# Kernel optimization log

Hardware: AMD Instinct MI355X
Metric: run time of the kernel (lower is better)

The kernel has to match this reference:

```python
import jax, jax.numpy as jnp
import numpy as np

B, N = 2048, 1024
ATOL, RTOL = 1e-6, 1e-3
MAX_STEPS = 40   # static bound on adaptive DOPRI5 steps over t in [0, 1]
DT0 = 0.1
T1 = 1.0

# Dormand-Prince 5(4) error coefficients (b5 - b4)
E1 = 71.0 / 57600.0
E3 = -71.0 / 16695.0
E4 = 71.0 / 1920.0
E5 = -17253.0 / 339200.0
E6 = 22.0 / 525.0
E7 = -1.0 / 40.0


def _dopri5_to_t1(f, y0):
    """Adaptive Dormand-Prince RK45 from t=0 to t=1 with a static step budget."""
    def body(carry, _):
        t, y, dt = carry
        done = t >= (T1 - 1e-7)
        h = jnp.where(done, jnp.float32(0.0), jnp.minimum(dt, T1 - t))
        k1 = f(y)
        k2 = f(y + h * (0.2 * k1))
        k3 = f(y + h * (3.0/40.0 * k1 + 9.0/40.0 * k2))
        k4 = f(y + h * (44.0/45.0 * k1 - 56.0/15.0 * k2 + 32.0/9.0 * k3))
        k5 = f(y + h * (19372.0/6561.0 * k1 - 25360.0/2187.0 * k2
                        + 64448.0/6561.0 * k3 - 212.0/729.0 * k4))
        k6 = f(y + h * (9017.0/3168.0 * k1 - 355.0/33.0 * k2 + 46732.0/5247.0 * k3
                        + 49.0/176.0 * k4 - 5103.0/18656.0 * k5))
        y5 = y + h * (35.0/384.0 * k1 + 500.0/1113.0 * k3 + 125.0/192.0 * k4
                      - 2187.0/6784.0 * k5 + 11.0/84.0 * k6)
        k7 = f(y5)  # FSAL stage, used only for error estimate here
        err = h * (E1*k1 + E3*k3 + E4*k4 + E5*k5 + E6*k6 + E7*k7)
        scale = ATOL + RTOL * jnp.maximum(jnp.abs(y), jnp.abs(y5))
        enorm = jnp.sqrt(jnp.mean(jnp.square(err / scale)))
        enorm = jnp.maximum(enorm, jnp.float32(1e-10))
        accept = enorm <= 1.0
        step_ok = jnp.logical_and(accept, jnp.logical_not(done))
        t_new = jnp.where(step_ok, t + h, t)
        y_new = jnp.where(step_ok, y5, y)
        factor = jnp.clip(0.9 * enorm ** (-0.2), 0.2, 5.0)
        dt_new = jnp.where(done, dt, dt * factor)
        return (t_new, y_new, dt_new), None

    carry0 = (jnp.float32(0.0), y0, jnp.float32(DT0))
    (_, y_final, _), _ = jax.lax.scan(jax.checkpoint(body), carry0, None, length=MAX_STEPS)
    return y_final


def setup_inputs() -> dict:
    key = jax.random.key(0)
    k1, k2, k3, k4 = jax.random.split(key, 4)
    inputs = jax.random.normal(k1, (B, N), dtype=jnp.float32)
    prev_state = jax.random.normal(k2, (B, N), dtype=jnp.float32)
    # keras initializers: tau='ones', weights/input_weights=RandomNormal(stddev=0.05), bias='zeros'
    tau = jnp.ones((N,), dtype=jnp.float32)
    weight_matrix = 0.05 * jax.random.normal(k3, (N, N), dtype=jnp.float32)
    input_weights = 0.05 * jax.random.normal(k4, (N,), dtype=jnp.float32)
    bias = jnp.zeros((N,), dtype=jnp.float32)
    return {"inputs": inputs, "prev_state": prev_state, "tau": tau,
            "weight_matrix": weight_matrix, "input_weights": input_weights, "bias": bias}


def reference(inputs, prev_state, tau, weight_matrix, input_weights, bias):
    drive = inputs * input_weights  # [B, N], constant over the integration
    inv_tau = 1.0 / tau

    def ode_fn(y):  # autonomous: dx/dt = (1/tau) * (-x + W @ tanh(x + b) + u * w_in)
        act = jnp.tanh(y + bias)
        rec = jnp.einsum('ij,bj->bi', weight_matrix, act)
        return inv_tau * (-y + rec + drive)

    new_state = _dopri5_to_t1(ode_fn, prev_state)
    return new_state
```

## Files before the change

### kernel.cpp

```cpp
#include <hip/hip_runtime.h>
#include <math.h>


typedef float f4 __attribute__((ext_vector_type(4)));
typedef float f32x4 __attribute__((ext_vector_type(4)));
typedef _Float16 half8v __attribute__((ext_vector_type(8)));
typedef _Float16 half2v __attribute__((ext_vector_type(2)));
typedef unsigned long long u64;

#define AS1 __attribute__((address_space(1)))
#define AS3 __attribute__((address_space(3)))

#define NBLK 256
#define NTHR 512

#define E1c (71.0f / 57600.0f)
#define E3c (-71.0f / 16695.0f)
#define E4c (71.0f / 1920.0f)
#define E5c (-17253.0f / 339200.0f)
#define E6c (22.0f / 525.0f)
#define E7c (-1.0f / 40.0f)

#define ALDI(p) __hip_atomic_load((p), __ATOMIC_ACQUIRE, __HIP_MEMORY_SCOPE_AGENT)
#define ASTI(p, v) __hip_atomic_store((p), (v), __ATOMIC_RELEASE, __HIP_MEMORY_SCOPE_AGENT)
#define ALD64(p) __hip_atomic_load((p), __ATOMIC_ACQUIRE, __HIP_MEMORY_SCOPE_AGENT)
#define AST64(p, v) __hip_atomic_store((p), (v), __ATOMIC_RELEASE, __HIP_MEMORY_SCOPE_AGENT)

__global__ void k_zero(u64* pk, int* flg) {
  int i = blockIdx.x * blockDim.x + threadIdx.x;
  if (i < 2048) pk[i] = 0ull;
  if (i < 4096) flg[i] = 0;
}

__device__ __forceinline__ float ftanh(float x) {
  x = fminf(fmaxf(x, -9.0f), 9.0f);
  float e = __expf(2.0f * x);
  return (e - 1.0f) / (e + 1.0f);
}

__global__ void k_prep(const float* __restrict__ W, _Float16* __restrict__ Wf) {
  int i = blockIdx.x * blockDim.x + threadIdx.x;
  int l = i & 63, kb = (i >> 6) & 31, ct = i >> 11;
  const float* src = W + (size_t)(ct * 16 + (l & 15)) * 1024 + kb * 32 + (l >> 4) * 8;
  half8v o;
#pragma unroll
  for (int j = 0; j < 8; ++j) o[j] = (_Float16)src[j];
  *(half8v*)(Wf + ((size_t)i << 3)) = o;
}

__device__ __forceinline__ f32x4 mfma(half8v a, half8v b, f32x4 c) {
  return __builtin_amdgcn_mfma_f32_16x16x32_f16(a, b, c, 0, 0, 0);
}

__device__ __forceinline__ void gemm_half(const char* Ak, const _Float16* wfk,
                                          int l, int rot, f32x4 acc[4]) {
  const int r = l & 15, lk = l >> 4, r7 = l & 7;
  const char* arow = Ak + r * 1024;
  half8v bA[4], bB[4];
#pragma unroll
  for (int ci = 0; ci < 4; ++ci)
    bA[ci] = *(const half8v*)(wfk + (ci << 14) + (rot << 9));
#pragma unroll 1
  for (int it = 0; it < 16; it += 2) {
    const int kb0 = (it + rot) & 15;
    const int kb1 = (it + 1 + rot) & 15;
    const int kb2 = (it + 2 + rot) & 15;
    half8v a0 = *(const half8v*)(arow + ((((kb0 << 2) | lk) ^ r7) << 4));
#pragma unroll
    for (int ci = 0; ci < 4; ++ci)
      bB[ci] = *(const half8v*)(wfk + (ci << 14) + (kb1 << 9));
#pragma unroll
    for (int ci = 0; ci < 4; ++ci) acc[ci] = mfma(a0, bA[ci], acc[ci]);
    half8v a1 = *(const half8v*)(arow + ((((kb1 << 2) | lk) ^ r7) << 4));
#pragma unroll
    for (int ci = 0; ci < 4; ++ci)
      bA[ci] = *(const half8v*)(wfk + (ci << 14) + (kb2 << 9));
#pragma unroll
    for (int ci = 0; ci < 4; ++ci) acc[ci] = mfma(a1, bB[ci], acc[ci]);
  }
}

__device__ __forceinline__ void exch_gemm(
    char* Ab, _Float16* gxm, const _Float16* gxp,
    int* flg, int bid, int partner, int pcnt,
    const _Float16* wfbW, int colHalf, int l, int tid, int rot, f32x4 acc[4]) {
  __syncthreads();
  {
    const char* src = Ab + colHalf * 16384;
    char* dst = (char*)gxm;
#pragma unroll
    for (int u = 0; u < 2; ++u) {
      int off = (u * 512 + tid) * 16;
      f4 v = *(const f4*)(src + off);
      *(f4*)(dst + off) = v;
    }
  }
  __syncthreads();
  if (tid == 0) ASTI(&flg[bid * 16], pcnt);
#pragma unroll
  for (int ci = 0; ci < 4; ++ci)
#pragma unroll
    for (int q = 0; q < 4; ++q) acc[ci][q] = 0.0f;
  gemm_half(Ab + colHalf * 16384, wfbW + (colHalf << 13), l, rot, acc);
  if (tid == 0) {
    while (ALDI(&flg[partner * 16]) < pcnt) __builtin_amdgcn_s_sleep(1);
  }
  __syncthreads();
#pragma unroll
  for (int u = 0; u < 2; ++u) {
    int off = (u * 512 + tid) * 16;
    __builtin_amdgcn_global_load_lds(
        (const AS1 void*)((const char*)gxp + off),
        (AS3 void*)(Ab + (colHalf ^ 1) * 16384 + off), 16, 0, 0);
  }
  __syncthreads();
  gemm_half(Ab + (colHalf ^ 1) * 16384, wfbW + ((colHalf ^ 1) << 13), l, rot, acc);
}

template <int S>
__device__ __forceinline__ void stage_epi(
    const f32x4 acc[4], float h,
    float* yT, float* ysT, const half2v* dh,
    half2v* k1h, half2v* k2h, half2v* k3h, half2v* k4h, half2v* k5h, half2v* eh,
    const float* itau4, const float* bias4,
    char* Ab, int colHalf, int wv, int l, float* errAcc) {
  const int lk4 = (l >> 4) * 4, lr16 = l & 15;
#pragma unroll
  for (int ci = 0; ci < 4; ++ci) {
#pragma unroll
    for (int q = 0; q < 4; ++q) {
      const int e = ci * 4 + q;
      float yv = yT[e * NTHR];
      float ks;
      if constexpr (S == 1) {
        ks = (float)k1h[e >> 1][e & 1];
      } else {
        ks = itau4[ci] * ((float)dh[e >> 1][e & 1] + acc[ci][q] - ysT[e * NTHR]);
      }
      float nys;
      if constexpr (S == 1) {
        eh[e >> 1][e & 1] = (_Float16)(E1c * ks);
        nys = yv + h * (0.2f * ks);
      } else if constexpr (S == 2) {
        k2h[e >> 1][e & 1] = (_Float16)ks;
        float k1 = (float)k1h[e >> 1][e & 1];
        nys = yv + h * ((3.0f / 40.0f) * k1 + (9.0f / 40.0f) * ks);
      } else if constexpr (S == 3) {
        k3h[e >> 1][e & 1] = (_Float16)ks;
        eh[e >> 1][e & 1] = (_Float16)((float)eh[e >> 1][e & 1] + E3c * ks);
        float k1 = (float)k1h[e >> 1][e & 1], k2 = (float)k2h[e >> 1][e & 1];
        nys = yv + h * ((44.0f / 45.0f) * k1 + (-56.0f / 15.0f) * k2 + (32.0f / 9.0f) * ks);
      } else if constexpr (S == 4) {
        k4h[e >> 1][e & 1] = (_Float16)ks;
        eh[e >> 1][e & 1] = (_Float16)((float)eh[e >> 1][e & 1] + E4c * ks);
        float k1 = (float)k1h[e >> 1][e & 1], k2 = (float)k2h[e >> 1][e & 1];
        float k3 = (float)k3h[e >> 1][e & 1];
        nys = yv + h * ((19372.0f / 6561.0f) * k1 + (-25360.0f / 2187.0f) * k2 +
                        (64448.0f / 6561.0f) * k3 + (-212.0f / 729.0f) * ks);
      } else if constexpr (S == 5) {
        k5h[e >> 1][e & 1] = (_Float16)ks;
        eh[e >> 1][e & 1] = (_Float16)((float)eh[e >> 1][e & 1] + E5c * ks);
        float k1 = (float)k1h[e >> 1][e & 1], k2 = (float)k2h[e >> 1][e & 1];
        float k3 = (float)k3h[e >> 1][e & 1], k4 = (float)k4h[e >> 1][e & 1];
        nys = yv + h * ((9017.0f / 3168.0f) * k1 + (-355.0f / 33.0f) * k2 +
                        (46732.0f / 5247.0f) * k3 + (49.0f / 176.0f) * k4 +
                        (-5103.0f / 18656.0f) * ks);
      } else if constexpr (S == 6) {
        eh[e >> 1][e & 1] = (_Float16)((float)eh[e >> 1][e & 1] + E6c * ks);
        float k1 = (float)k1h[e >> 1][e & 1];
        float k3 = (float)k3h[e >> 1][e & 1], k4 = (float)k4h[e >> 1][e & 1];
        float k5 = (float)k5h[e >> 1][e & 1];
        nys = yv + h * ((35.0f / 384.0f) * k1 + (500.0f / 1113.0f) * k3 +
                        (125.0f / 192.0f) * k4 + (-2187.0f / 6784.0f) * k5 +
                        (11.0f / 84.0f) * ks);
      } else {
        k2h[e >> 1][e & 1] = (_Float16)ks;
        float ev = h * ((float)eh[e >> 1][e & 1] + E7c * ks);
        float sc = 1e-6f + 1e-3f * fmaxf(fabsf(yv), fabsf(ysT[e * NTHR]));
        float r = ev / sc;
        *errAcc += r * r;
        nys = 0.0f;
      }
      if constexpr (S <= 6) {
        ysT[e * NTHR] = nys;
        float av = ftanh(nys + bias4[ci]);
        int rowl = lk4 + q;
        int colp = wv * 64 + ci * 16 + lr16;
        *(_Float16*)(Ab + colHalf * 16384 + rowl * 1024 +
                     ((((colp >> 3) ^ (rowl & 7)) << 4)) + (colp & 7) * 2) =
            (_Float16)av;
      }
    }
  }
}

__global__ __launch_bounds__(NTHR) void k_ode(
    const float* __restrict__ inp, const float* __restrict__ prev,
    const float* __restrict__ tau, const float* __restrict__ iw,
    const float* __restrict__ bias, const _Float16* __restrict__ Wf,
    _Float16* __restrict__ gx, float* __restrict__ out,
    u64* __restrict__ pk, int* __restrict__ flg) {
  __shared__ _Float16 actL[2][2][16][512];
  __shared__ float yL[16 * NTHR];
  __shared__ float ysL[16 * NTHR];
  __shared__ float sm[256];
  __shared__ float wsum[8];
  __shared__ float bc;

  const int tid = (int)threadIdx.x, bid = (int)blockIdx.x;
  const int l = tid & 63, wv = tid >> 6;
  const int lr16 = l & 15, lk4 = (l >> 4) * 4;
  const int rowGroup = (bid & 7) | ((bid >> 4) << 3);
  const int colHalf = (bid >> 3) & 1;
  const int partner = bid ^ 8;
  const int rbase = rowGroup * 16;
  const int rot = (bid >> 3) & 15;
  char* A0 = (char*)&actL[0][0][0][0];
  char* A1 = (char*)&actL[1][0][0][0];
  float* yT = yL + tid;
  float* ysT = ysL + tid;
  const _Float16* wfbW = Wf + ((size_t)(colHalf * 32 + wv * 4) << 14) + (l << 3);
  _Float16* gxm[2];
  const _Float16* gxp[2];
#pragma unroll
  for (int b = 0; b < 2; ++b) {
    gxm[b] = gx + (size_t)(b * 256 + bid) * 8192;
    gxp[b] = gx + (size_t)(b * 256 + partner) * 8192;
  }

  half2v dh[8], k1h[8], k2h[8], k3h[8], k4h[8], k5h[8], eh[8];
  float itau4[4], bias4[4];
#pragma unroll
  for (int ci = 0; ci < 4; ++ci) {
    int col = colHalf * 512 + wv * 64 + ci * 16 + lr16;
    itau4[ci] = 1.0f / tau[col];
    bias4[ci] = bias[col];
  }
#pragma unroll
  for (int ci = 0; ci < 4; ++ci)
#pragma unroll
    for (int q = 0; q < 4; ++q) {
      const int e = ci * 4 + q;
      int rowl = lk4 + q;
      int colp = wv * 64 + ci * 16 + lr16;
      int col = colHalf * 512 + colp;
      size_t off = (size_t)(rbase + rowl) * 1024 + col;
      float yv = prev[off];
      yT[e * NTHR] = yv;
      ysT[e * NTHR] = yv;
      dh[e >> 1][e & 1] = (_Float16)(inp[off] * iw[col]);
      float av = ftanh(yv + bias4[ci]);
      *(_Float16*)(A1 + colHalf * 16384 + rowl * 1024 +
                   ((((colp >> 3) ^ (rowl & 7)) << 4)) + (colp & 7) * 2) =
          (_Float16)av;
    }

  f32x4 acc[4];
  int pcnt = 1;
  exch_gemm(A1, gxm[1], gxp[1], flg, bid, partner, pcnt,
            wfbW, colHalf, l, tid, rot, acc);
#pragma unroll
  for (int ci = 0; ci < 4; ++ci)
#pragma unroll
    for (int q = 0; q < 4; ++q) {
      const int e = ci * 4 + q;
      k1h[e >> 1][e & 1] =
          (_Float16)(itau4[ci] * ((float)dh[e >> 1][e & 1] + acc[ci][q] - yT[e * NTHR]));
    }

  float t = 0.0f, dtv = 0.1f;
#pragma unroll 1
  for (int s = 0; s < 40; ++s) {
    if (t >= 1.0f - 1e-7f) break;
    const float h = fminf(dtv, 1.0f - t);

    stage_epi<1>(acc, h, yT, ysT, dh, k1h, k2h, k3h, k4h, k5h, eh, itau4, bias4,
                 A0, colHalf, wv, l, nullptr);
    exch_gemm(A0, gxm[0], gxp[0], flg, bid, partner, ++pcnt,
              wfbW, colHalf, l, tid, rot, acc);
    stage_epi<2>(acc, h, yT, ysT, dh, k1h, k2h, k3h, k4h, k5h, eh, itau4, bias4,
                 A1, colHalf, wv, l, nullptr);
    exch_gemm(A1, gxm[1], gxp[1], flg, bid, partner, ++pcnt,
              wfbW, colHalf, l, tid, rot, acc);
    stage_epi<3>(acc, h, yT, ysT, dh, k1h, k2h, k3h, k4h, k5h, eh, itau4, bias4,
                 A0, colHalf, wv, l, nullptr);
    exch_gemm(A0, gxm[0], gxp[0], flg, bid, partner, ++pcnt,
              wfbW, colHalf, l, tid, rot, acc);
    stage_epi<4>(acc, h, yT, ysT, dh, k1h, k2h, k3h, k4h, k5h, eh, itau4, bias4,
                 A1, colHalf, wv, l, nullptr);
    exch_gemm(A1, gxm[1], gxp[1], flg, bid, partner, ++pcnt,
              wfbW, colHalf, l, tid, rot, acc);
    stage_epi<5>(acc, h, yT, ysT, dh, k1h, k2h, k3h, k4h, k5h, eh, itau4, bias4,
                 A0, colHalf, wv, l, nullptr);
    exch_gemm(A0, gxm[0], gxp[0], flg, bid, partner, ++pcnt,
              wfbW, colHalf, l, tid, rot, acc);
    stage_epi<6>(acc, h, yT, ysT, dh, k1h, k2h, k3h, k4h, k5h, eh, itau4, bias4,
                 A1, colHalf, wv, l, nullptr);
    exch_gemm(A1, gxm[1], gxp[1], flg, bid, partner, ++pcnt,
              wfbW, colHalf, l, tid, rot, acc);
    float errAcc = 0.0f;
    stage_epi<7>(acc, h, yT, ysT, dh, k1h, k2h, k3h, k4h, k5h, eh, itau4, bias4,
                 nullptr, colHalf, wv, l, &errAcc);

#pragma unroll
    for (int o = 32; o > 0; o >>= 1) errAcc += __shfl_down(errAcc, o, 64);
    if (l == 0) wsum[wv] = errAcc;
    __syncthreads();
    float sblk = 0.0f;
    if (tid == 0) {
#pragma unroll
      for (int w = 0; w < 8; ++w) sblk += wsum[w];
    }
    const u64 ep = (u64)(s + 2);
    const int slot = (int)(ep & 1);
    if (tid == 0)
      AST64(&pk[bid * 8 + slot], (ep << 32) | (u64)__float_as_uint(sblk));
    if (tid < 256) {
      u64 v;
      do { v = ALD64(&pk[tid * 8 + slot]); } while ((v >> 32) < ep);
      sm[tid] = __uint_as_float((unsigned)v);
    }
    __syncthreads();
    if (tid < 64) {
      float a = sm[tid] + sm[tid + 64] + sm[tid + 128] + sm[tid + 192];
#pragma unroll
      for (int o = 1; o < 64; o <<= 1) a += __shfl_xor(a, o, 64);
      if (tid == 0) bc = a;
    }
    __syncthreads();
    float sd = bc;

    float enorm = fmaxf(sqrtf(sd / 2097152.0f), 1e-10f);
    if (enorm <= 1.0f) {
      t = t + h;
#pragma unroll
      for (int e = 0; e < 16; ++e) yT[e * NTHR] = ysT[e * NTHR];
#pragma unroll
      for (int i = 0; i < 8; ++i) k1h[i] = k2h[i];
    }
    float factor = fminf(fmaxf(0.9f * powf(enorm, -0.2f), 0.2f), 5.0f);
    dtv = dtv * factor;
  }

#pragma unroll
  for (int ci = 0; ci < 4; ++ci)
#pragma unroll
    for (int q = 0; q < 4; ++q) {
      const int e = ci * 4 + q;
      int rowl = lk4 + q;
      int col = colHalf * 512 + wv * 64 + ci * 16 + lr16;
      out[(size_t)(rbase + rowl) * 1024 + col] = yT[e * NTHR];
    }
}

extern "C" void kernel_launch(void* const* d_in, const int* in_sizes, int n_in,
                              void* d_out, int out_size, void* d_ws, size_t ws_size,
                              hipStream_t stream) {
  const float* inp = (const float*)d_in[0];
  const float* prev = (const float*)d_in[1];
  const float* tau = (const float*)d_in[2];
  const float* W = (const float*)d_in[3];
  const float* iw = (const float*)d_in[4];
  const float* bias = (const float*)d_in[5];
  float* out = (float*)d_out;

  char* ws = (char*)d_ws;
  const size_t MB = 1024 * 1024;
  u64* pk = (u64*)ws;
  int* flg = (int*)(ws + 16384);
  _Float16* Wf = (_Float16*)(ws + 64 * 1024);
  _Float16* gx = (_Float16*)(ws + 64 * 1024 + 2 * MB);

  k_zero<<<8, 512, 0, stream>>>(pk, flg);
  k_prep<<<512, 256, 0, stream>>>(W, Wf);
  k_ode<<<NBLK, NTHR, 0, stream>>>(inp, prev, tau, iw, bias, Wf, gx, out, pk, flg);
}
```

Measured before the change: 584.5 us.

## Double threads per block, halve per-wave columns, keep ODE state in registers

Raises the block size from 512 to 1024 threads, so each wave owns 32 output columns (2 MFMA tiles) instead of 64. The y and ys state arrays move from LDS into registers, and the exchange copy loops drop to one vector per thread. The aim is more waves in flight to hide latency in the serial per-stage GEMM and epilogue, plus fewer LDS accesses. In exchange, every wave now loads its own A-operand reads, so LDS traffic per MFMA roughly doubles, and the 1024-thread launch tightens the per-thread register budget.

```diff
diff --git a/kernel.cpp b/kernel.cpp
--- a/kernel.cpp
+++ b/kernel.cpp
@@ -12,7 +12,7 @@
 #define AS3 __attribute__((address_space(3)))
 
 #define NBLK 256
-#define NTHR 512
+#define NTHR 1024
 
 #define E1c (71.0f / 57600.0f)
 #define E3c (-71.0f / 16695.0f)
@@ -53,12 +53,12 @@
 }
 
 __device__ __forceinline__ void gemm_half(const char* Ak, const _Float16* wfk,
-                                          int l, int rot, f32x4 acc[4]) {
+                                          int l, int rot, f32x4 acc[2]) {
   const int r = l & 15, lk = l >> 4, r7 = l & 7;
   const char* arow = Ak + r * 1024;
-  half8v bA[4], bB[4];
-#pragma unroll
-  for (int ci = 0; ci < 4; ++ci)
+  half8v bA[2], bB[2];
+#pragma unroll
+  for (int ci = 0; ci < 2; ++ci)
     bA[ci] = *(const half8v*)(wfk + (ci << 14) + (rot << 9));
 #pragma unroll 1
   for (int it = 0; it < 16; it += 2) {
@@ -67,48 +67,42 @@
     const int kb2 = (it + 2 + rot) & 15;
     half8v a0 = *(const half8v*)(arow + ((((kb0 << 2) | lk) ^ r7) << 4));
 #pragma unroll
-    for (int ci = 0; ci < 4; ++ci)
+    for (int ci = 0; ci < 2; ++ci)
       bB[ci] = *(const half8v*)(wfk + (ci << 14) + (kb1 << 9));
 #pragma unroll
-    for (int ci = 0; ci < 4; ++ci) acc[ci] = mfma(a0, bA[ci], acc[ci]);
+    for (int ci = 0; ci < 2; ++ci) acc[ci] = mfma(a0, bA[ci], acc[ci]);
     half8v a1 = *(const half8v*)(arow + ((((kb1 << 2) | lk) ^ r7) << 4));
 #pragma unroll
-    for (int ci = 0; ci < 4; ++ci)
+    for (int ci = 0; ci < 2; ++ci)
       bA[ci] = *(const half8v*)(wfk + (ci << 14) + (kb2 << 9));
 #pragma unroll
-    for (int ci = 0; ci < 4; ++ci) acc[ci] = mfma(a1, bB[ci], acc[ci]);
+    for (int ci = 0; ci < 2; ++ci) acc[ci] = mfma(a1, bB[ci], acc[ci]);
   }
 }
 
 __device__ __forceinline__ void exch_gemm(
     char* Ab, _Float16* gxm, const _Float16* gxp,
     int* flg, int bid, int partner, int pcnt,
-    const _Float16* wfbW, int colHalf, int l, int tid, int rot, f32x4 acc[4]) {
+    const _Float16* wfbW, int colHalf, int l, int tid, int rot, f32x4 acc[2]) {
   __syncthreads();
   {
     const char* src = Ab + colHalf * 16384;
     char* dst = (char*)gxm;
-#pragma unroll
-    for (int u = 0; u < 2; ++u) {
-      int off = (u * 512 + tid) * 16;
-      f4 v = *(const f4*)(src + off);
-      *(f4*)(dst + off) = v;
-    }
+    int off = tid * 16;
+    f4 v = *(const f4*)(src + off);
+    *(f4*)(dst + off) = v;
   }
   __syncthreads();
   if (tid == 0) ASTI(&flg[bid * 16], pcnt);
-#pragma unroll
-  for (int ci = 0; ci < 4; ++ci)
-#pragma unroll
-    for (int q = 0; q < 4; ++q) acc[ci][q] = 0.0f;
+  acc[0] = (f32x4){0.0f, 0.0f, 0.0f, 0.0f};
+  acc[1] = (f32x4){0.0f, 0.0f, 0.0f, 0.0f};
   gemm_half(Ab + colHalf * 16384, wfbW + (colHalf << 13), l, rot, acc);
   if (tid == 0) {
     while (ALDI(&flg[partner * 16]) < pcnt) __builtin_amdgcn_s_sleep(1);
   }
   __syncthreads();
-#pragma unroll
-  for (int u = 0; u < 2; ++u) {
-    int off = (u * 512 + tid) * 16;
+  {
+    int off = tid * 16;
     __builtin_amdgcn_global_load_lds(
         (const AS1 void*)((const char*)gxp + off),
         (AS3 void*)(Ab + (colHalf ^ 1) * 16384 + off), 16, 0, 0);
@@ -119,23 +113,23 @@
 
 template <int S>
 __device__ __forceinline__ void stage_epi(
-    const f32x4 acc[4], float h,
-    float* yT, float* ysT, const half2v* dh,
+    const f32x4 acc[2], float h,
+    float* y, float* ys, const half2v* dh,
     half2v* k1h, half2v* k2h, half2v* k3h, half2v* k4h, half2v* k5h, half2v* eh,
-    const float* itau4, const float* bias4,
+    const float* itau2, const float* bias2,
     char* Ab, int colHalf, int wv, int l, float* errAcc) {
   const int lk4 = (l >> 4) * 4, lr16 = l & 15;
 #pragma unroll
-  for (int ci = 0; ci < 4; ++ci) {
+  for (int ci = 0; ci < 2; ++ci) {
 #pragma unroll
     for (int q = 0; q < 4; ++q) {
       const int e = ci * 4 + q;
-      float yv = yT[e * NTHR];
+      float yv = y[e];
       float ks;
       if constexpr (S == 1) {
         ks = (float)k1h[e >> 1][e & 1];
       } else {
-        ks = itau4[ci] * ((float)dh[e >> 1][e & 1] + acc[ci][q] - ysT[e * NTHR]);
+        ks = itau2[ci] * ((float)dh[e >> 1][e & 1] + acc[ci][q] - ys[e]);
       }
       float nys;
       if constexpr (S == 1) {
@@ -176,16 +170,16 @@
       } else {
         k2h[e >> 1][e & 1] = (_Float16)ks;
         float ev = h * ((float)eh[e >> 1][e & 1] + E7c * ks);
-        float sc = 1e-6f + 1e-3f * fmaxf(fabsf(yv), fabsf(ysT[e * NTHR]));
+        float sc = 1e-6f + 1e-3f * fmaxf(fabsf(yv), fabsf(ys[e]));
         float r = ev / sc;
         *errAcc += r * r;
         nys = 0.0f;
       }
       if constexpr (S <= 6) {
-        ysT[e * NTHR] = nys;
-        float av = ftanh(nys + bias4[ci]);
+        ys[e] = nys;
+        float av = ftanh(nys + bias2[ci]);
         int rowl = lk4 + q;
-        int colp = wv * 64 + ci * 16 + lr16;
+        int colp = wv * 32 + ci * 16 + lr16;
         *(_Float16*)(Ab + colHalf * 16384 + rowl * 1024 +
                      ((((colp >> 3) ^ (rowl & 7)) << 4)) + (colp & 7) * 2) =
             (_Float16)av;
@@ -201,10 +195,8 @@
     _Float16* __restrict__ gx, float* __restrict__ out,
     u64* __restrict__ pk, int* __restrict__ flg) {
   __shared__ _Float16 actL[2][2][16][512];
-  __shared__ float yL[16 * NTHR];
-  __shared__ float ysL[16 * NTHR];
   __shared__ float sm[256];
-  __shared__ float wsum[8];
+  __shared__ float wsum[16];
   __shared__ float bc;
 
   const int tid = (int)threadIdx.x, bid = (int)blockIdx.x;
@@ -217,9 +209,7 @@
   const int rot = (bid >> 3) & 15;
   char* A0 = (char*)&actL[0][0][0][0];
   char* A1 = (char*)&actL[1][0][0][0];
-  float* yT = yL + tid;
-  float* ysT = ysL + tid;
-  const _Float16* wfbW = Wf + ((size_t)(colHalf * 32 + wv * 4) << 14) + (l << 3);
+  const _Float16* wfbW = Wf + ((size_t)(colHalf * 32 + wv * 2) << 14) + (l << 3);
   _Float16* gxm[2];
   const _Float16* gxp[2];
 #pragma unroll
@@ -228,44 +218,45 @@
     gxp[b] = gx + (size_t)(b * 256 + partner) * 8192;
   }
 
-  half2v dh[8], k1h[8], k2h[8], k3h[8], k4h[8], k5h[8], eh[8];
-  float itau4[4], bias4[4];
-#pragma unroll
-  for (int ci = 0; ci < 4; ++ci) {
-    int col = colHalf * 512 + wv * 64 + ci * 16 + lr16;
-    itau4[ci] = 1.0f / tau[col];
-    bias4[ci] = bias[col];
-  }
-#pragma unroll
-  for (int ci = 0; ci < 4; ++ci)
+  float y[8], ysr[8];
+  half2v dh[4], k1h[4], k2h[4], k3h[4], k4h[4], k5h[4], eh[4];
+  float itau2[2], bias2[2];
+#pragma unroll
+  for (int ci = 0; ci < 2; ++ci) {
+    int col = colHalf * 512 + wv * 32 + ci * 16 + lr16;
+    itau2[ci] = 1.0f / tau[col];
+    bias2[ci] = bias[col];
+  }
+#pragma unroll
+  for (int ci = 0; ci < 2; ++ci)
 #pragma unroll
     for (int q = 0; q < 4; ++q) {
       const int e = ci * 4 + q;
       int rowl = lk4 + q;
-      int colp = wv * 64 + ci * 16 + lr16;
+      int colp = wv * 32 + ci * 16 + lr16;
       int col = colHalf * 512 + colp;
       size_t off = (size_t)(rbase + rowl) * 1024 + col;
       float yv = prev[off];
-      yT[e * NTHR] = yv;
-      ysT[e * NTHR] = yv;
+      y[e] = yv;
+      ysr[e] = yv;
       dh[e >> 1][e & 1] = (_Float16)(inp[off] * iw[col]);
-      float av = ftanh(yv + bias4[ci]);
+      float av = ftanh(yv + bias2[ci]);
       *(_Float16*)(A1 + colHalf * 16384 + rowl * 1024 +
                    ((((colp >> 3) ^ (rowl & 7)) << 4)) + (colp & 7) * 2) =
           (_Float16)av;
     }
 
-  f32x4 acc[4];
+  f32x4 acc[2];
   int pcnt = 1;
   exch_gemm(A1, gxm[1], gxp[1], flg, bid, partner, pcnt,
             wfbW, colHalf, l, tid, rot, acc);
 #pragma unroll
-  for (int ci = 0; ci < 4; ++ci)
+  for (int ci = 0; ci < 2; ++ci)
 #pragma unroll
     for (int q = 0; q < 4; ++q) {
       const int e = ci * 4 + q;
       k1h[e >> 1][e & 1] =
-          (_Float16)(itau4[ci] * ((float)dh[e >> 1][e & 1] + acc[ci][q] - yT[e * NTHR]));
+          (_Float16)(itau2[ci] * ((float)dh[e >> 1][e & 1] + acc[ci][q] - y[e]));
     }
 
   float t = 0.0f, dtv = 0.1f;
@@ -274,32 +265,32 @@
     if (t >= 1.0f - 1e-7f) break;
     const float h = fminf(dtv, 1.0f - t);
 
-    stage_epi<1>(acc, h, yT, ysT, dh, k1h, k2h, k3h, k4h, k5h, eh, itau4, bias4,
+    stage_epi<1>(acc, h, y, ysr, dh, k1h, k2h, k3h, k4h, k5h, eh, itau2, bias2,
                  A0, colHalf, wv, l, nullptr);
     exch_gemm(A0, gxm[0], gxp[0], flg, bid, partner, ++pcnt,
               wfbW, colHalf, l, tid, rot, acc);
-    stage_epi<2>(acc, h, yT, ysT, dh, k1h, k2h, k3h, k4h, k5h, eh, itau4, bias4,
+    stage_epi<2>(acc, h, y, ysr, dh, k1h, k2h, k3h, k4h, k5h, eh, itau2, bias2,
                  A1, colHalf, wv, l, nullptr);
     exch_gemm(A1, gxm[1], gxp[1], flg, bid, partner, ++pcnt,
               wfbW, colHalf, l, tid, rot, acc);
-    stage_epi<3>(acc, h, yT, ysT, dh, k1h, k2h, k3h, k4h, k5h, eh, itau4, bias4,
+    stage_epi<3>(acc, h, y, ysr, dh, k1h, k2h, k3h, k4h, k5h, eh, itau2, bias2,
                  A0, colHalf, wv, l, nullptr);
     exch_gemm(A0, gxm[0], gxp[0], flg, bid, partner, ++pcnt,
               wfbW, colHalf, l, tid, rot, acc);
-    stage_epi<4>(acc, h, yT, ysT, dh, k1h, k2h, k3h, k4h, k5h, eh, itau4, bias4,
+    stage_epi<4>(acc, h, y, ysr, dh, k1h, k2h, k3h, k4h, k5h, eh, itau2, bias2,
                  A1, colHalf, wv, l, nullptr);
     exch_gemm(A1, gxm[1], gxp[1], flg, bid, partner, ++pcnt,
               wfbW, colHalf, l, tid, rot, acc);
-    stage_epi<5>(acc, h, yT, ysT, dh, k1h, k2h, k3h, k4h, k5h, eh, itau4, bias4,
+    stage_epi<5>(acc, h, y, ysr, dh, k1h, k2h, k3h, k4h, k5h, eh, itau2, bias2,
                  A0, colHalf, wv, l, nullptr);
     exch_gemm(A0, gxm[0], gxp[0], flg, bid, partner, ++pcnt,
               wfbW, colHalf, l, tid, rot, acc);
-    stage_epi<6>(acc, h, yT, ysT, dh, k1h, k2h, k3h, k4h, k5h, eh, itau4, bias4,
+    stage_epi<6>(acc, h, y, ysr, dh, k1h, k2h, k3h, k4h, k5h, eh, itau2, bias2,
                  A1, colHalf, wv, l, nullptr);
     exch_gemm(A1, gxm[1], gxp[1], flg, bid, partner, ++pcnt,
               wfbW, colHalf, l, tid, rot, acc);
     float errAcc = 0.0f;
-    stage_epi<7>(acc, h, yT, ysT, dh, k1h, k2h, k3h, k4h, k5h, eh, itau4, bias4,
+    stage_epi<7>(acc, h, y, ysr, dh, k1h, k2h, k3h, k4h, k5h, eh, itau2, bias2,
                  nullptr, colHalf, wv, l, &errAcc);
 
 #pragma unroll
@@ -309,7 +300,7 @@
     float sblk = 0.0f;
     if (tid == 0) {
 #pragma unroll
-      for (int w = 0; w < 8; ++w) sblk += wsum[w];
+      for (int w = 0; w < 16; ++w) sblk += wsum[w];
     }
     const u64 ep = (u64)(s + 2);
     const int slot = (int)(ep & 1);
@@ -334,22 +325,22 @@
     if (enorm <= 1.0f) {
       t = t + h;
 #pragma unroll
-      for (int e = 0; e < 16; ++e) yT[e * NTHR] = ysT[e * NTHR];
-#pragma unroll
-      for (int i = 0; i < 8; ++i) k1h[i] = k2h[i];
+      for (int e = 0; e < 8; ++e) y[e] = ysr[e];
+#pragma unroll
+      for (int i = 0; i < 4; ++i) k1h[i] = k2h[i];
     }
     float factor = fminf(fmaxf(0.9f * powf(enorm, -0.2f), 0.2f), 5.0f);
     dtv = dtv * factor;
   }
 
 #pragma unroll
-  for (int ci = 0; ci < 4; ++ci)
+  for (int ci = 0; ci < 2; ++ci)
 #pragma unroll
     for (int q = 0; q < 4; ++q) {
       const int e = ci * 4 + q;
       int rowl = lk4 + q;
-      int col = colHalf * 512 + wv * 64 + ci * 16 + lr16;
-      out[(size_t)(rbase + rowl) * 1024 + col] = yT[e * NTHR];
+      int col = colHalf * 512 + wv * 32 + ci * 16 + lr16;
+      out[(size_t)(rbase + rowl) * 1024 + col] = y[e];
     }
 }
 
```

Result: slower. 645.5 us (+10.4%).

## Repartition ODE blocks into 32-row by 256-column tiles with four-way activation exchange

Applied to the files above, without the earlier changes.

Each block now owns 32 batch rows and a quarter of the output columns (256) instead of 16 rows and half the columns. Activations are exchanged among four blocks per row group through global scratch with per-block flags, rather than between a pair. The GEMM reuses each loaded weight fragment across two row tiles (2x2 accumulators), halving weight traffic per row. The cost is waiting on three partner flags per stage, which adds more cross-block synchronization per stage.

```diff
diff --git a/kernel.cpp b/kernel.cpp
--- a/kernel.cpp
+++ b/kernel.cpp
@@ -52,143 +52,162 @@
   return __builtin_amdgcn_mfma_f32_16x16x32_f16(a, b, c, 0, 0, 0);
 }
 
-__device__ __forceinline__ void gemm_half(const char* Ak, const _Float16* wfk,
-                                          int l, int rot, f32x4 acc[4]) {
-  const int r = l & 15, lk = l >> 4, r7 = l & 7;
-  const char* arow = Ak + r * 1024;
-  half8v bA[4], bB[4];
-#pragma unroll
-  for (int ci = 0; ci < 4; ++ci)
-    bA[ci] = *(const half8v*)(wfk + (ci << 14) + (rot << 9));
+__device__ __forceinline__ void gemm_quarter(const char* Aq,
+                                             const _Float16* wfW, int kq,
+                                             int l, int rot, f32x4 acc[2][2]) {
+  const int lr = l & 15, lk = l >> 4, r7 = l & 7;
+  const char* ar0 = Aq + lr * 512;
+  const char* ar1 = Aq + (16 + lr) * 512;
+  const _Float16* wk = wfW + (kq << 12);
+  half8v bA[2], bB[2];
+  bA[0] = *(const half8v*)(wk + (rot << 9));
+  bA[1] = *(const half8v*)(wk + (1 << 14) + (rot << 9));
 #pragma unroll 1
-  for (int it = 0; it < 16; it += 2) {
-    const int kb0 = (it + rot) & 15;
-    const int kb1 = (it + 1 + rot) & 15;
-    const int kb2 = (it + 2 + rot) & 15;
-    half8v a0 = *(const half8v*)(arow + ((((kb0 << 2) | lk) ^ r7) << 4));
-#pragma unroll
-    for (int ci = 0; ci < 4; ++ci)
-      bB[ci] = *(const half8v*)(wfk + (ci << 14) + (kb1 << 9));
-#pragma unroll
-    for (int ci = 0; ci < 4; ++ci) acc[ci] = mfma(a0, bA[ci], acc[ci]);
-    half8v a1 = *(const half8v*)(arow + ((((kb1 << 2) | lk) ^ r7) << 4));
-#pragma unroll
-    for (int ci = 0; ci < 4; ++ci)
-      bA[ci] = *(const half8v*)(wfk + (ci << 14) + (kb2 << 9));
-#pragma unroll
-    for (int ci = 0; ci < 4; ++ci) acc[ci] = mfma(a1, bB[ci], acc[ci]);
+  for (int it = 0; it < 8; it += 2) {
+    const int k0 = (it + rot) & 7;
+    const int k1 = (it + 1 + rot) & 7;
+    const int k2 = (it + 2 + rot) & 7;
+    half8v a00 = *(const half8v*)(ar0 + ((((k0 << 2) | lk) ^ r7) << 4));
+    half8v a01 = *(const half8v*)(ar1 + ((((k0 << 2) | lk) ^ r7) << 4));
+    bB[0] = *(const half8v*)(wk + (k1 << 9));
+    bB[1] = *(const half8v*)(wk + (1 << 14) + (k1 << 9));
+    acc[0][0] = mfma(a00, bA[0], acc[0][0]);
+    acc[0][1] = mfma(a00, bA[1], acc[0][1]);
+    acc[1][0] = mfma(a01, bA[0], acc[1][0]);
+    acc[1][1] = mfma(a01, bA[1], acc[1][1]);
+    half8v a10 = *(const half8v*)(ar0 + ((((k1 << 2) | lk) ^ r7) << 4));
+    half8v a11 = *(const half8v*)(ar1 + ((((k1 << 2) | lk) ^ r7) << 4));
+    bA[0] = *(const half8v*)(wk + (k2 << 9));
+    bA[1] = *(const half8v*)(wk + (1 << 14) + (k2 << 9));
+    acc[0][0] = mfma(a10, bB[0], acc[0][0]);
+    acc[0][1] = mfma(a10, bB[1], acc[0][1]);
+    acc[1][0] = mfma(a11, bB[0], acc[1][0]);
+    acc[1][1] = mfma(a11, bB[1], acc[1][1]);
   }
 }
 
 __device__ __forceinline__ void exch_gemm(
-    char* Ab, _Float16* gxm, const _Float16* gxp,
-    int* flg, int bid, int partner, int pcnt,
-    const _Float16* wfbW, int colHalf, int l, int tid, int rot, f32x4 acc[4]) {
+    char* Ab, char* gxB, int* flg, int bid, int rg, int quarter,
+    int pcnt, const _Float16* wfW, int l, int tid, int rot, f32x4 acc[2][2]) {
   __syncthreads();
   {
-    const char* src = Ab + colHalf * 16384;
-    char* dst = (char*)gxm;
-#pragma unroll
-    for (int u = 0; u < 2; ++u) {
-      int off = (u * 512 + tid) * 16;
-      f4 v = *(const f4*)(src + off);
-      *(f4*)(dst + off) = v;
-    }
+    int off = tid * 16;
+    const char* src = Ab + quarter * 16384;
+    f4 v0 = *(const f4*)(src + off);
+    f4 v1 = *(const f4*)(src + off + 8192);
+    char* dst = gxB + (size_t)bid * 16384;
+    *(f4*)(dst + off) = v0;
+    *(f4*)(dst + off + 8192) = v1;
   }
   __syncthreads();
   if (tid == 0) ASTI(&flg[bid * 16], pcnt);
 #pragma unroll
-  for (int ci = 0; ci < 4; ++ci)
-#pragma unroll
-    for (int q = 0; q < 4; ++q) acc[ci][q] = 0.0f;
-  gemm_half(Ab + colHalf * 16384, wfbW + (colHalf << 13), l, rot, acc);
-  if (tid == 0) {
-    while (ALDI(&flg[partner * 16]) < pcnt) __builtin_amdgcn_s_sleep(1);
+  for (int a = 0; a < 2; ++a)
+#pragma unroll
+    for (int b = 0; b < 2; ++b)
+#pragma unroll
+      for (int q = 0; q < 4; ++q) acc[a][b][q] = 0.0f;
+  gemm_quarter(Ab + quarter * 16384, wfW, quarter, l, rot, acc);
+  if (tid < 3) {
+    int pq = (quarter + 1 + tid) & 3;
+    int pbid = (pq << 6) | rg;
+    while (ALDI(&flg[pbid * 16]) < pcnt) __builtin_amdgcn_s_sleep(1);
   }
   __syncthreads();
 #pragma unroll
-  for (int u = 0; u < 2; ++u) {
-    int off = (u * 512 + tid) * 16;
-    __builtin_amdgcn_global_load_lds(
-        (const AS1 void*)((const char*)gxp + off),
-        (AS3 void*)(Ab + (colHalf ^ 1) * 16384 + off), 16, 0, 0);
+  for (int j = 1; j < 4; ++j) {
+    int pq = (quarter + j) & 3;
+    int pbid = (pq << 6) | rg;
+    const char* src = gxB + (size_t)pbid * 16384;
+    int off = tid * 16;
+    __builtin_amdgcn_global_load_lds((const AS1 void*)(src + off),
+                                     (AS3 void*)(Ab + pq * 16384 + off), 16, 0, 0);
+    __builtin_amdgcn_global_load_lds((const AS1 void*)(src + off + 8192),
+                                     (AS3 void*)(Ab + pq * 16384 + off + 8192), 16, 0, 0);
   }
   __syncthreads();
-  gemm_half(Ab + (colHalf ^ 1) * 16384, wfbW + ((colHalf ^ 1) << 13), l, rot, acc);
+#pragma unroll
+  for (int j = 1; j < 4; ++j) {
+    int pq = (quarter + j) & 3;
+    gemm_quarter(Ab + pq * 16384, wfW, pq, l, rot, acc);
+  }
 }
 
 template <int S>
 __device__ __forceinline__ void stage_epi(
-    const f32x4 acc[4], float h,
+    const f32x4 acc[2][2], float h,
     float* yT, float* ysT, const half2v* dh,
     half2v* k1h, half2v* k2h, half2v* k3h, half2v* k4h, half2v* k5h, half2v* eh,
-    const float* itau4, const float* bias4,
-    char* Ab, int colHalf, int wv, int l, float* errAcc) {
-  const int lk4 = (l >> 4) * 4, lr16 = l & 15;
-#pragma unroll
-  for (int ci = 0; ci < 4; ++ci) {
-#pragma unroll
-    for (int q = 0; q < 4; ++q) {
-      const int e = ci * 4 + q;
-      float yv = yT[e * NTHR];
-      float ks;
-      if constexpr (S == 1) {
-        ks = (float)k1h[e >> 1][e & 1];
-      } else {
-        ks = itau4[ci] * ((float)dh[e >> 1][e & 1] + acc[ci][q] - ysT[e * NTHR]);
-      }
-      float nys;
-      if constexpr (S == 1) {
-        eh[e >> 1][e & 1] = (_Float16)(E1c * ks);
-        nys = yv + h * (0.2f * ks);
-      } else if constexpr (S == 2) {
-        k2h[e >> 1][e & 1] = (_Float16)ks;
-        float k1 = (float)k1h[e >> 1][e & 1];
-        nys = yv + h * ((3.0f / 40.0f) * k1 + (9.0f / 40.0f) * ks);
-      } else if constexpr (S == 3) {
-        k3h[e >> 1][e & 1] = (_Float16)ks;
-        eh[e >> 1][e & 1] = (_Float16)((float)eh[e >> 1][e & 1] + E3c * ks);
-        float k1 = (float)k1h[e >> 1][e & 1], k2 = (float)k2h[e >> 1][e & 1];
-        nys = yv + h * ((44.0f / 45.0f) * k1 + (-56.0f / 15.0f) * k2 + (32.0f / 9.0f) * ks);
-      } else if constexpr (S == 4) {
-        k4h[e >> 1][e & 1] = (_Float16)ks;
-        eh[e >> 1][e & 1] = (_Float16)((float)eh[e >> 1][e & 1] + E4c * ks);
-        float k1 = (float)k1h[e >> 1][e & 1], k2 = (float)k2h[e >> 1][e & 1];
-        float k3 = (float)k3h[e >> 1][e & 1];
-        nys = yv + h * ((19372.0f / 6561.0f) * k1 + (-25360.0f / 2187.0f) * k2 +
-                        (64448.0f / 6561.0f) * k3 + (-212.0f / 729.0f) * ks);
-      } else if constexpr (S == 5) {
-        k5h[e >> 1][e & 1] = (_Float16)ks;
-        eh[e >> 1][e & 1] = (_Float16)((float)eh[e >> 1][e & 1] + E5c * ks);
-        float k1 = (float)k1h[e >> 1][e & 1], k2 = (float)k2h[e >> 1][e & 1];
-        float k3 = (float)k3h[e >> 1][e & 1], k4 = (float)k4h[e >> 1][e & 1];
-        nys = yv + h * ((9017.0f / 3168.0f) * k1 + (-355.0f / 33.0f) * k2 +
-                        (46732.0f / 5247.0f) * k3 + (49.0f / 176.0f) * k4 +
-                        (-5103.0f / 18656.0f) * ks);
-      } else if constexpr (S == 6) {
-        eh[e >> 1][e & 1] = (_Float16)((float)eh[e >> 1][e & 1] + E6c * ks);
-        float k1 = (float)k1h[e >> 1][e & 1];
-        float k3 = (float)k3h[e >> 1][e & 1], k4 = (float)k4h[e >> 1][e & 1];
-        float k5 = (float)k5h[e >> 1][e & 1];
-        nys = yv + h * ((35.0f / 384.0f) * k1 + (500.0f / 1113.0f) * k3 +
-                        (125.0f / 192.0f) * k4 + (-2187.0f / 6784.0f) * k5 +
-                        (11.0f / 84.0f) * ks);
-      } else {
-        k2h[e >> 1][e & 1] = (_Float16)ks;
-        float ev = h * ((float)eh[e >> 1][e & 1] + E7c * ks);
-        float sc = 1e-6f + 1e-3f * fmaxf(fabsf(yv), fabsf(ysT[e * NTHR]));
-        float r = ev / sc;
-        *errAcc += r * r;
-        nys = 0.0f;
-      }
-      if constexpr (S <= 6) {
-        ysT[e * NTHR] = nys;
-        float av = ftanh(nys + bias4[ci]);
-        int rowl = lk4 + q;
-        int colp = wv * 64 + ci * 16 + lr16;
-        *(_Float16*)(Ab + colHalf * 16384 + rowl * 1024 +
-                     ((((colp >> 3) ^ (rowl & 7)) << 4)) + (colp & 7) * 2) =
-            (_Float16)av;
+    const float* itau2, const float* bias2,
+    char* Ab, int quarter, int wv, int l, float* errAcc) {
+  const int lk4 = ((l >> 4) & 3) * 4, lr16 = l & 15;
+#pragma unroll
+  for (int rt = 0; rt < 2; ++rt) {
+#pragma unroll
+    for (int ci = 0; ci < 2; ++ci) {
+#pragma unroll
+      for (int qq = 0; qq < 4; ++qq) {
+        const int e = rt * 8 + ci * 4 + qq;
+        float yv = yT[e * NTHR];
+        float ks;
+        if constexpr (S == 1) {
+          ks = (float)k1h[e >> 1][e & 1];
+        } else {
+          ks = itau2[ci] * ((float)dh[e >> 1][e & 1] + acc[rt][ci][qq] - ysT[e * NTHR]);
+        }
+        float nys;
+        if constexpr (S == 1) {
+          eh[e >> 1][e & 1] = (_Float16)(E1c * ks);
+          nys = yv + h * (0.2f * ks);
+        } else if constexpr (S == 2) {
+          k2h[e >> 1][e & 1] = (_Float16)ks;
+          float k1 = (float)k1h[e >> 1][e & 1];
+          nys = yv + h * ((3.0f / 40.0f) * k1 + (9.0f / 40.0f) * ks);
+        } else if constexpr (S == 3) {
+          k3h[e >> 1][e & 1] = (_Float16)ks;
+          eh[e >> 1][e & 1] = (_Float16)((float)eh[e >> 1][e & 1] + E3c * ks);
+          float k1 = (float)k1h[e >> 1][e & 1], k2 = (float)k2h[e >> 1][e & 1];
+          nys = yv + h * ((44.0f / 45.0f) * k1 + (-56.0f / 15.0f) * k2 + (32.0f / 9.0f) * ks);
+        } else if constexpr (S == 4) {
+          k4h[e >> 1][e & 1] = (_Float16)ks;
+          eh[e >> 1][e & 1] = (_Float16)((float)eh[e >> 1][e & 1] + E4c * ks);
+          float k1 = (float)k1h[e >> 1][e & 1], k2 = (float)k2h[e >> 1][e & 1];
+          float k3 = (float)k3h[e >> 1][e & 1];
+          nys = yv + h * ((19372.0f / 6561.0f) * k1 + (-25360.0f / 2187.0f) * k2 +
+                          (64448.0f / 6561.0f) * k3 + (-212.0f / 729.0f) * ks);
+        } else if constexpr (S == 5) {
+          k5h[e >> 1][e & 1] = (_Float16)ks;
+          eh[e >> 1][e & 1] = (_Float16)((float)eh[e >> 1][e & 1] + E5c * ks);
+          float k1 = (float)k1h[e >> 1][e & 1], k2 = (float)k2h[e >> 1][e & 1];
+          float k3 = (float)k3h[e >> 1][e & 1], k4 = (float)k4h[e >> 1][e & 1];
+          nys = yv + h * ((9017.0f / 3168.0f) * k1 + (-355.0f / 33.0f) * k2 +
+                          (46732.0f / 5247.0f) * k3 + (49.0f / 176.0f) * k4 +
+                          (-5103.0f / 18656.0f) * ks);
+        } else if constexpr (S == 6) {
+          eh[e >> 1][e & 1] = (_Float16)((float)eh[e >> 1][e & 1] + E6c * ks);
+          float k1 = (float)k1h[e >> 1][e & 1];
+          float k3 = (float)k3h[e >> 1][e & 1], k4 = (float)k4h[e >> 1][e & 1];
+          float k5 = (float)k5h[e >> 1][e & 1];
+          nys = yv + h * ((35.0f / 384.0f) * k1 + (500.0f / 1113.0f) * k3 +
+                          (125.0f / 192.0f) * k4 + (-2187.0f / 6784.0f) * k5 +
+                          (11.0f / 84.0f) * ks);
+        } else {
+          k2h[e >> 1][e & 1] = (_Float16)ks;
+          float ev = h * ((float)eh[e >> 1][e & 1] + E7c * ks);
+          float sc = 1e-6f + 1e-3f * fmaxf(fabsf(yv), fabsf(ysT[e * NTHR]));
+          float r = ev / sc;
+          *errAcc += r * r;
+          nys = 0.0f;
+        }
+        if constexpr (S <= 6) {
+          ysT[e * NTHR] = nys;
+          float av = ftanh(nys + bias2[ci]);
+          int rowl = rt * 16 + lk4 + qq;
+          int colp = wv * 32 + ci * 16 + lr16;
+          *(_Float16*)(Ab + quarter * 16384 + rowl * 512 +
+                       ((((colp >> 3) ^ (rowl & 7)) << 4)) + (colp & 7) * 2) =
+              (_Float16)av;
+        }
       }
     }
   }
@@ -198,9 +217,9 @@
     const float* __restrict__ inp, const float* __restrict__ prev,
     const float* __restrict__ tau, const float* __restrict__ iw,
     const float* __restrict__ bias, const _Float16* __restrict__ Wf,
-    _Float16* __restrict__ gx, float* __restrict__ out,
+    char* __restrict__ gx, float* __restrict__ out,
     u64* __restrict__ pk, int* __restrict__ flg) {
-  __shared__ _Float16 actL[2][2][16][512];
+  __shared__ _Float16 actL[4][32][256];
   __shared__ float yL[16 * NTHR];
   __shared__ float ysL[16 * NTHR];
   __shared__ float sm[256];
@@ -209,64 +228,60 @@
 
   const int tid = (int)threadIdx.x, bid = (int)blockIdx.x;
   const int l = tid & 63, wv = tid >> 6;
-  const int lr16 = l & 15, lk4 = (l >> 4) * 4;
-  const int rowGroup = (bid & 7) | ((bid >> 4) << 3);
-  const int colHalf = (bid >> 3) & 1;
-  const int partner = bid ^ 8;
-  const int rbase = rowGroup * 16;
-  const int rot = (bid >> 3) & 15;
-  char* A0 = (char*)&actL[0][0][0][0];
-  char* A1 = (char*)&actL[1][0][0][0];
+  const int lr16 = l & 15, lk4 = ((l >> 4) & 3) * 4;
+  const int rg = bid & 63;
+  const int quarter = bid >> 6;
+  const int rbase = rg * 32;
+  const int colBase = quarter * 256;
+  const int rot = ((rg >> 3) + quarter * 2) & 7;
+  char* Ab = (char*)&actL[0][0][0];
   float* yT = yL + tid;
   float* ysT = ysL + tid;
-  const _Float16* wfbW = Wf + ((size_t)(colHalf * 32 + wv * 4) << 14) + (l << 3);
-  _Float16* gxm[2];
-  const _Float16* gxp[2];
-#pragma unroll
-  for (int b = 0; b < 2; ++b) {
-    gxm[b] = gx + (size_t)(b * 256 + bid) * 8192;
-    gxp[b] = gx + (size_t)(b * 256 + partner) * 8192;
-  }
+  const _Float16* wfW = Wf + ((size_t)(quarter * 16 + wv * 2) << 14) + (l << 3);
+  char* gxB[2] = {gx, gx + (size_t)NBLK * 16384};
 
   half2v dh[8], k1h[8], k2h[8], k3h[8], k4h[8], k5h[8], eh[8];
-  float itau4[4], bias4[4];
-#pragma unroll
-  for (int ci = 0; ci < 4; ++ci) {
-    int col = colHalf * 512 + wv * 64 + ci * 16 + lr16;
-    itau4[ci] = 1.0f / tau[col];
-    bias4[ci] = bias[col];
-  }
-#pragma unroll
-  for (int ci = 0; ci < 4; ++ci)
-#pragma unroll
-    for (int q = 0; q < 4; ++q) {
-      const int e = ci * 4 + q;
-      int rowl = lk4 + q;
-      int colp = wv * 64 + ci * 16 + lr16;
-      int col = colHalf * 512 + colp;
-      size_t off = (size_t)(rbase + rowl) * 1024 + col;
-      float yv = prev[off];
-      yT[e * NTHR] = yv;
-      ysT[e * NTHR] = yv;
-      dh[e >> 1][e & 1] = (_Float16)(inp[off] * iw[col]);
-      float av = ftanh(yv + bias4[ci]);
-      *(_Float16*)(A1 + colHalf * 16384 + rowl * 1024 +
-                   ((((colp >> 3) ^ (rowl & 7)) << 4)) + (colp & 7) * 2) =
-          (_Float16)av;
-    }
-
-  f32x4 acc[4];
+  float itau2[2], bias2[2];
+#pragma unroll
+  for (int ci = 0; ci < 2; ++ci) {
+    int col = colBase + wv * 32 + ci * 16 + lr16;
+    itau2[ci] = 1.0f / tau[col];
+    bias2[ci] = bias[col];
+  }
+#pragma unroll
+  for (int rt = 0; rt < 2; ++rt)
+#pragma unroll
+    for (int ci = 0; ci < 2; ++ci)
+#pragma unroll
+      for (int qq = 0; qq < 4; ++qq) {
+        const int e = rt * 8 + ci * 4 + qq;
+        int rowl = rt * 16 + lk4 + qq;
+        int colp = wv * 32 + ci * 16 + lr16;
+        int col = colBase + colp;
+        size_t off = (size_t)(rbase + rowl) * 1024 + col;
+        float yv = prev[off];
+        yT[e * NTHR] = yv;
+        ysT[e * NTHR] = yv;
+        dh[e >> 1][e & 1] = (_Float16)(inp[off] * iw[col]);
+        float av = ftanh(yv + bias2[ci]);
+        *(_Float16*)(Ab + quarter * 16384 + rowl * 512 +
+                     ((((colp >> 3) ^ (rowl & 7)) << 4)) + (colp & 7) * 2) =
+            (_Float16)av;
+      }
+
+  f32x4 acc[2][2];
   int pcnt = 1;
-  exch_gemm(A1, gxm[1], gxp[1], flg, bid, partner, pcnt,
-            wfbW, colHalf, l, tid, rot, acc);
-#pragma unroll
-  for (int ci = 0; ci < 4; ++ci)
-#pragma unroll
-    for (int q = 0; q < 4; ++q) {
-      const int e = ci * 4 + q;
-      k1h[e >> 1][e & 1] =
-          (_Float16)(itau4[ci] * ((float)dh[e >> 1][e & 1] + acc[ci][q] - yT[e * NTHR]));
-    }
+  exch_gemm(Ab, gxB[1], flg, bid, rg, quarter, pcnt, wfW, l, tid, rot, acc);
+#pragma unroll
+  for (int rt = 0; rt < 2; ++rt)
+#pragma unroll
+    for (int ci = 0; ci < 2; ++ci)
+#pragma unroll
+      for (int qq = 0; qq < 4; ++qq) {
+        const int e = rt * 8 + ci * 4 + qq;
+        k1h[e >> 1][e & 1] =
+            (_Float16)(itau2[ci] * ((float)dh[e >> 1][e & 1] + acc[rt][ci][qq] - yT[e * NTHR]));
+      }
 
   float t = 0.0f, dtv = 0.1f;
 #pragma unroll 1
@@ -274,33 +289,27 @@
     if (t >= 1.0f - 1e-7f) break;
     const float h = fminf(dtv, 1.0f - t);
 
-    stage_epi<1>(acc, h, yT, ysT, dh, k1h, k2h, k3h, k4h, k5h, eh, itau4, bias4,
-                 A0, colHalf, wv, l, nullptr);
-    exch_gemm(A0, gxm[0], gxp[0], flg, bid, partner, ++pcnt,
-              wfbW, colHalf, l, tid, rot, acc);
-    stage_epi<2>(acc, h, yT, ysT, dh, k1h, k2h, k3h, k4h, k5h, eh, itau4, bias4,
-                 A1, colHalf, wv, l, nullptr);
-    exch_gemm(A1, gxm[1], gxp[1], flg, bid, partner, ++pcnt,
-              wfbW, colHalf, l, tid, rot, acc);
-    stage_epi<3>(acc, h, yT, ysT, dh, k1h, k2h, k3h, k4h, k5h, eh, itau4, bias4,
-                 A0, colHalf, wv, l, nullptr);
-    exch_gemm(A0, gxm[0], gxp[0], flg, bid, partner, ++pcnt,
-              wfbW, colHalf, l, tid, rot, acc);
-    stage_epi<4>(acc, h, yT, ysT, dh, k1h, k2h, k3h, k4h, k5h, eh, itau4, bias4,
-                 A1, colHalf, wv, l, nullptr);
-    exch_gemm(A1, gxm[1], gxp[1], flg, bid, partner, ++pcnt,
-              wfbW, colHalf, l, tid, rot, acc);
-    stage_epi<5>(acc, h, yT, ysT, dh, k1h, k2h, k3h, k4h, k5h, eh, itau4, bias4,
-                 A0, colHalf, wv, l, nullptr);
-    exch_gemm(A0, gxm[0], gxp[0], flg, bid, partner, ++pcnt,
-              wfbW, colHalf, l, tid, rot, acc);
-    stage_epi<6>(acc, h, yT, ysT, dh, k1h, k2h, k3h, k4h, k5h, eh, itau4, bias4,
-                 A1, colHalf, wv, l, nullptr);
-    exch_gemm(A1, gxm[1], gxp[1], flg, bid, partner, ++pcnt,
-              wfbW, colHalf, l, tid, rot, acc);
+    stage_epi<1>(acc, h, yT, ysT, dh, k1h, k2h, k3h, k4h, k5h, eh, itau2, bias2,
+                 Ab, quarter, wv, l, nullptr);
+    ++pcnt; exch_gemm(Ab, gxB[pcnt & 1], flg, bid, rg, quarter, pcnt, wfW, l, tid, rot, acc);
+    stage_epi<2>(acc, h, yT, ysT, dh, k1h, k2h, k3h, k4h, k5h, eh, itau2, bias2,
+                 Ab, quarter, wv, l, nullptr);
+    ++pcnt; exch_gemm(Ab, gxB[pcnt & 1], flg, bid, rg, quarter, pcnt, wfW, l, tid, rot, acc);
+    stage_epi<3>(acc, h, yT, ysT, dh, k1h, k2h, k3h, k4h, k5h, eh, itau2, bias2,
+                 Ab, quarter, wv, l, nullptr);
+    ++pcnt; exch_gemm(Ab, gxB[pcnt & 1], flg, bid, rg, quarter, pcnt, wfW, l, tid, rot, acc);
+    stage_epi<4>(acc, h, yT, ysT, dh, k1h, k2h, k3h, k4h, k5h, eh, itau2, bias2,
+                 Ab, quarter, wv, l, nullptr);
+    ++pcnt; exch_gemm(Ab, gxB[pcnt & 1], flg, bid, rg, quarter, pcnt, wfW, l, tid, rot, acc);
+    stage_epi<5>(acc, h, yT, ysT, dh, k1h, k2h, k3h, k4h, k5h, eh, itau2, bias2,
+                 Ab, quarter, wv, l, nullptr);
+    ++pcnt; exch_gemm(Ab, gxB[pcnt & 1], flg, bid, rg, quarter, pcnt, wfW, l, tid, rot, acc);
+    stage_epi<6>(acc, h, yT, ysT, dh, k1h, k2h, k3h, k4h, k5h, eh, itau2, bias2,
+                 Ab, quarter, wv, l, nullptr);
+    ++pcnt; exch_gemm(Ab, gxB[pcnt & 1], flg, bid, rg, quarter, pcnt, wfW, l, tid, rot, acc);
     float errAcc = 0.0f;
-    stage_epi<7>(acc, h, yT, ysT, dh, k1h, k2h, k3h, k4h, k5h, eh, itau4, bias4,
-                 nullptr, colHalf, wv, l, &errAcc);
+    stage_epi<7>(acc, h, yT, ysT, dh, k1h, k2h, k3h, k4h, k5h, eh, itau2, bias2,
+                 nullptr, quarter, wv, l, &errAcc);
 
 #pragma unroll
     for (int o = 32; o > 0; o >>= 1) errAcc += __shfl_down(errAcc, o, 64);
@@ -343,14 +352,16 @@
   }
 
 #pragma unroll
-  for (int ci = 0; ci < 4; ++ci)
-#pragma unroll
-    for (int q = 0; q < 4; ++q) {
-      const int e = ci * 4 + q;
-      int rowl = lk4 + q;
-      int col = colHalf * 512 + wv * 64 + ci * 16 + lr16;
-      out[(size_t)(rbase + rowl) * 1024 + col] = yT[e * NTHR];
-    }
+  for (int rt = 0; rt < 2; ++rt)
+#pragma unroll
+    for (int ci = 0; ci < 2; ++ci)
+#pragma unroll
+      for (int qq = 0; qq < 4; ++qq) {
+        const int e = rt * 8 + ci * 4 + qq;
+        int rowl = rt * 16 + lk4 + qq;
+        int col = colBase + wv * 32 + ci * 16 + lr16;
+        out[(size_t)(rbase + rowl) * 1024 + col] = yT[e * NTHR];
+      }
 }
 
 extern "C" void kernel_launch(void* const* d_in, const int* in_sizes, int n_in,
@@ -369,7 +380,7 @@
   u64* pk = (u64*)ws;
   int* flg = (int*)(ws + 16384);
   _Float16* Wf = (_Float16*)(ws + 64 * 1024);
-  _Float16* gx = (_Float16*)(ws + 64 * 1024 + 2 * MB);
+  char* gx = ws + 64 * 1024 + 2 * MB;
 
   k_zero<<<8, 512, 0, stream>>>(pk, flg);
   k_prep<<<512, 256, 0, stream>>>(W, Wf);
```

Result: faster. 512.8 us, median of 2 (-12.3%).
